# Kernel optimization log

Measured on AMD Instinct MI355X. Metric: run time of the kernel, lower is better.

The kernel has to match this reference:

```python
import jax, jax.numpy as jnp
import numpy as np

WS = 16      # window_size
HEADS = 8    # num_heads
EPS = 1e-5   # LayerNorm eps (torch default)


def setup_inputs() -> dict:
    key = jax.random.key(0)
    ks = jax.random.split(key, 7)
    C = 256
    x = jax.random.normal(ks[0], (8, C, 128, 128), dtype=jnp.float32)
    # LayerNorm params (torch init: weight=1, bias=0)
    ln_w = jnp.ones((C,), jnp.float32)
    ln_b = jnp.zeros((C,), jnp.float32)
    # MultiheadAttention in_proj (3C x C) and out_proj (C x C), xavier-ish scale
    s = 1.0 / np.sqrt(C)
    w_qkv = jax.random.uniform(ks[1], (3 * C, C), jnp.float32, -s, s)
    b_qkv = jnp.zeros((3 * C,), jnp.float32)
    w_out = jax.random.uniform(ks[2], (C, C), jnp.float32, -s, s)
    b_out = jnp.zeros((C,), jnp.float32)
    return {"x": x, "ln_w": ln_w, "ln_b": ln_b, "w_qkv": w_qkv,
            "b_qkv": b_qkv, "w_out": w_out, "b_out": b_out}


def _layernorm(x, w, b):
    mu = jnp.mean(x, axis=-1, keepdims=True)
    var = jnp.mean(jnp.square(x - mu), axis=-1, keepdims=True)
    return (x - mu) * jax.lax.rsqrt(var + EPS) * w + b


def reference(x, ln_w, ln_b, w_qkv, b_qkv, w_out, b_out):
    B, C, H, W = x.shape
    pad_h = (WS - H % WS) % WS
    pad_w = (WS - W % WS) % WS
    if pad_h or pad_w:
        x_p = jnp.pad(x, ((0, 0), (0, 0), (0, pad_h), (0, pad_w)))
    else:
        x_p = x
    nH, nW = x_p.shape[2] // WS, x_p.shape[3] // WS
    T = WS * WS
    # window partition: [B,C,H,W] -> [B*nH*nW, T, C]
    win = x_p.reshape(B, C, nH, WS, nW, WS)
    win = win.transpose(0, 2, 4, 3, 5, 1).reshape(B * nH * nW, T, C)

    xn = _layernorm(win, ln_w, ln_b)
    # QKV projection: [N,T,3C]
    qkv = jnp.einsum('ntc,dc->ntd', xn, w_qkv) + b_qkv
    q, k, v = jnp.split(qkv, 3, axis=-1)
    hd = C // HEADS
    N = win.shape[0]
    q = q.reshape(N, T, HEADS, hd).transpose(0, 2, 1, 3)  # [N,h,T,hd]
    k = k.reshape(N, T, HEADS, hd).transpose(0, 2, 1, 3)
    v = v.reshape(N, T, HEADS, hd).transpose(0, 2, 1, 3)
    scores = jnp.einsum('nhqd,nhkd->nhqk', q, k) / jnp.sqrt(jnp.asarray(hd, q.dtype))
    attn = jax.nn.softmax(scores, axis=-1)
    ctx = jnp.einsum('nhqk,nhkd->nhqd', attn, v)
    ctx = ctx.transpose(0, 2, 1, 3).reshape(N, T, C)
    attn_out = jnp.einsum('ntc,dc->ntd', ctx, w_out) + b_out

    win = win + attn_out
    # window reverse: [N,T,C] -> [B,C,H,W]
    out = win.reshape(B, nH, nW, WS, WS, C)
    out = out.transpose(0, 5, 1, 3, 2, 4).reshape(B, C, nH * WS, nW * WS)
    return out[:, :, :H, :W]
```

## Files before the change

### kernel.cpp

```cpp
#include <hip/hip_runtime.h>
#include <hip/hip_bf16.h>

#define CD    256
#define HW_   16384
#define WSZ   16
#define TT    256
#define NWIN  512
#define NHEADS 8
#define HDIM  32

typedef __hip_bfloat16 bf16;
typedef unsigned short ushort_t;
typedef __attribute__((ext_vector_type(8))) short bf16x8;
typedef __attribute__((ext_vector_type(4))) float f32x4;

__device__ __forceinline__ ushort_t f2bu(float v) {
    union { bf16 b; ushort_t u; } cv; cv.b = __float2bfloat16(v); return cv.u;
}

__device__ __forceinline__ float fexp2(float x) {
#if __has_builtin(__builtin_amdgcn_exp2f)
    return __builtin_amdgcn_exp2f(x);
#else
    return exp2f(x);
#endif
}

__global__ __launch_bounds__(256)
void convw_kernel(const float* __restrict__ wq, const float* __restrict__ wo,
                  bf16* __restrict__ wqb, bf16* __restrict__ wob)
{
    int i = blockIdx.x * 256 + threadIdx.x;
    if (i < 3 * CD * CD) wqb[i] = __float2bfloat16(wq[i]);
    int j = i - 3 * CD * CD;
    if (j >= 0 && j < CD * CD) wob[j] = __float2bfloat16(wo[j]);
}

__global__ __launch_bounds__(64)
void ln_kernel(const float* __restrict__ x, const float* __restrict__ lnw,
               const float* __restrict__ lnb, bf16* __restrict__ xn)
{
    __shared__ bf16 buf[64][72];

    const int blk = blockIdx.x;
    const int n = blk >> 2, q4 = blk & 3;
    const int t = q4 * 64 + threadIdx.x;
    const int b = n >> 6, r = n & 63;
    const int h0 = (r >> 3) * WSZ, w0 = (r & 7) * WSZ;
    const int ty = t >> 4, tx = t & 15;
    const float* px = x + (size_t)b * CD * HW_ + (size_t)(h0 + ty) * 128 + (w0 + tx);

    float s = 0.f, ss = 0.f;
    for (int c = 0; c < CD; ++c) { float v = px[(size_t)c * HW_]; s += v; ss += v * v; }
    const float mean = s * (1.f / CD);
    const float var  = ss * (1.f / CD) - mean * mean;
    const float rstd = rsqrtf(fmaxf(var, 0.f) + 1e-5f);

    const size_t gbase = ((size_t)n * TT + (size_t)q4 * 64) * CD;
    for (int cb = 0; cb < 4; ++cb) {
        __syncthreads();
        #pragma unroll
        for (int c8 = 0; c8 < 8; ++c8) {
            union { int4 q; ushort_t u[8]; } pk;
            #pragma unroll
            for (int j = 0; j < 8; ++j) {
                int c = cb * 64 + c8 * 8 + j;
                float v = px[(size_t)c * HW_];
                pk.u[j] = f2bu((v - mean) * rstd * lnw[c] + lnb[c]);
            }
            *(int4*)&buf[threadIdx.x][c8 * 8] = pk.q;
        }
        __syncthreads();
        for (int sl = threadIdx.x; sl < 512; sl += 64) {
            int row = sl >> 3, ch = sl & 7;
            *(int4*)&xn[gbase + (size_t)row * CD + cb * 64 + ch * 8] =
                *(const int4*)&buf[row][ch * 8];
        }
    }
}

__global__ __launch_bounds__(256, 2)
void attn_kernel(const bf16* __restrict__ xn, const bf16* __restrict__ wqb,
                 const float* __restrict__ bqkv, bf16* __restrict__ ctx)
{
    const int n = blockIdx.x, h = blockIdx.y;
    const int tid = threadIdx.x;
    const int wave = tid >> 6, lane = tid & 63;
    const int l16 = lane & 15, q16 = lane >> 4;

    __shared__ union {
        struct { bf16 xs[256][32]; bf16 ws[96][32]; } st;
        bf16 qp[256][40];
    } u;
    __shared__ bf16 ks[256][40];
    __shared__ bf16 vst[32][264];

    f32x4 acc[4][6];
    const f32x4 zero = {0.f, 0.f, 0.f, 0.f};
    #pragma unroll
    for (int mt = 0; mt < 4; ++mt)
        #pragma unroll
        for (int nt = 0; nt < 6; ++nt) acc[mt][nt] = zero;

    const size_t xbase = ((size_t)n * TT + tid) * CD;
    for (int kc = 0; kc < 8; ++kc) {
        __syncthreads();
        {
            const int4* src = (const int4*)(xn + xbase + kc * 32);
            int4* dst = (int4*)&u.st.xs[tid][0];
            #pragma unroll
            for (int i = 0; i < 4; ++i) dst[i] = src[i];
        }
        #pragma unroll
        for (int sl0 = 0; sl0 < 2; ++sl0) {
            int sl = sl0 * 256 + tid;
            if (sl < 384) {
                int row = sl >> 2, ch = sl & 3;
                int mat = row >> 5, j = row & 31;
                *(int4*)&u.st.ws[row][ch * 8] =
                    *(const int4*)(wqb + ((size_t)(mat * CD + h * HDIM + j)) * CD
                                   + (size_t)kc * 32 + ch * 8);
            }
        }
        __syncthreads();
        bf16x8 af[4], bg[6];
        #pragma unroll
        for (int mt = 0; mt < 4; ++mt)
            af[mt] = *(const bf16x8*)&u.st.xs[wave * 64 + mt * 16 + l16][q16 * 8];
        #pragma unroll
        for (int nt = 0; nt < 6; ++nt)
            bg[nt] = *(const bf16x8*)&u.st.ws[nt * 16 + l16][q16 * 8];
        #pragma unroll
        for (int mt = 0; mt < 4; ++mt)
            #pragma unroll
            for (int nt = 0; nt < 6; ++nt)
                acc[mt][nt] = __builtin_amdgcn_mfma_f32_16x16x32_bf16(
                                  af[mt], bg[nt], acc[mt][nt], 0, 0, 0);
    }
    __syncthreads();

    const float qscale2 = 0.2550348683f;
    #pragma unroll
    for (int nt = 0; nt < 6; ++nt) {
        const int mat = nt >> 1;
        const int j = ((nt & 1) << 4) | l16;
        const float bias = bqkv[mat * CD + h * HDIM + j];
        #pragma unroll
        for (int mt = 0; mt < 4; ++mt)
            #pragma unroll
            for (int rr = 0; rr < 4; ++rr) {
                int tok = wave * 64 + mt * 16 + q16 * 4 + rr;
                float v = acc[mt][nt][rr] + bias;
                if (mat == 0)      u.qp[tok][j] = __float2bfloat16(v * qscale2);
                else if (mat == 1) ks[tok][j]   = __float2bfloat16(v);
                else               vst[j][tok]  = __float2bfloat16(v);
            }
    }
    __syncthreads();

    bf16x8 aq[4];
    #pragma unroll
    for (int mt = 0; mt < 4; ++mt)
        aq[mt] = *(const bf16x8*)&u.qp[wave * 64 + mt * 16 + l16][q16 * 8];

    bf16x8 onesf;
    #pragma unroll
    for (int j = 0; j < 8; ++j) onesf[j] = (short)0x3F80;

    f32x4 acc_o[4][2];
    f32x4 acc_l[4];
    #pragma unroll
    for (int mt = 0; mt < 4; ++mt) {
        acc_o[mt][0] = zero; acc_o[mt][1] = zero; acc_l[mt] = zero;
    }

    for (int kc = 0; kc < 8; ++kc) {
        bf16x8 kb0 = *(const bf16x8*)&ks[kc * 32 + l16][q16 * 8];
        bf16x8 kb1 = *(const bf16x8*)&ks[kc * 32 + 16 + l16][q16 * 8];
        #pragma unroll
        for (int mt = 0; mt < 4; ++mt) {
            f32x4 sc0 = __builtin_amdgcn_mfma_f32_16x16x32_bf16(aq[mt], kb0, zero, 0, 0, 0);
            f32x4 sc1 = __builtin_amdgcn_mfma_f32_16x16x32_bf16(aq[mt], kb1, zero, 0, 0, 0);
            #pragma unroll
            for (int rr = 0; rr < 4; ++rr) {
                float p0 = fexp2(sc0[rr]);
                float p1 = fexp2(sc1[rr]);
                int row = wave * 64 + mt * 16 + q16 * 4 + rr;
                u.qp[row][l16]      = __float2bfloat16(p0);
                u.qp[row][16 + l16] = __float2bfloat16(p1);
            }
        }
        bf16x8 vb0 = *(const bf16x8*)&vst[l16][kc * 32 + q16 * 8];
        bf16x8 vb1 = *(const bf16x8*)&vst[16 + l16][kc * 32 + q16 * 8];
        #pragma unroll
        for (int mt = 0; mt < 4; ++mt) {
            bf16x8 ap = *(const bf16x8*)&u.qp[wave * 64 + mt * 16 + l16][q16 * 8];
            acc_o[mt][0] = __builtin_amdgcn_mfma_f32_16x16x32_bf16(ap, vb0, acc_o[mt][0], 0, 0, 0);
            acc_o[mt][1] = __builtin_amdgcn_mfma_f32_16x16x32_bf16(ap, vb1, acc_o[mt][1], 0, 0, 0);
            acc_l[mt]    = __builtin_amdgcn_mfma_f32_16x16x32_bf16(ap, onesf, acc_l[mt], 0, 0, 0);
        }
    }

    #pragma unroll
    for (int mt = 0; mt < 4; ++mt)
        #pragma unroll
        for (int rr = 0; rr < 4; ++rr) {
            const float inv_l = 1.f / acc_l[mt][rr];
            int tok = wave * 64 + mt * 16 + q16 * 4 + rr;
            size_t base = ((size_t)n * TT + tok) * CD + h * HDIM;
            ctx[base + l16]      = __float2bfloat16(acc_o[mt][0][rr] * inv_l);
            ctx[base + 16 + l16] = __float2bfloat16(acc_o[mt][1][rr] * inv_l);
        }
}

__global__ __launch_bounds__(256, 2)
void proj_kernel(const bf16* __restrict__ ctx, const bf16* __restrict__ wob,
                 const float* __restrict__ bout, const float* __restrict__ x,
                 float* __restrict__ out)
{
    const int mb = blockIdx.x, nb = blockIdx.y;
    const int tid = threadIdx.x;
    const int wave = tid >> 6, lane = tid & 63;
    const int l16 = lane & 15, q16 = lane >> 4;
    const int rowbase = (wave >> 1) * 64, colbase = (wave & 1) * 64;

    __shared__ union {
        struct { bf16 a[128][64]; bf16 b[128][64]; } st;
        bf16 c[128][129];
    } u;

    f32x4 acc[4][4];
    const f32x4 zero = {0.f, 0.f, 0.f, 0.f};
    #pragma unroll
    for (int mt = 0; mt < 4; ++mt)
        #pragma unroll
        for (int nt = 0; nt < 4; ++nt) acc[mt][nt] = zero;

    const size_t m0 = (size_t)mb * 128;
    for (int kc = 0; kc < 4; ++kc) {
        __syncthreads();
        #pragma unroll
        for (int p = 0; p < 4; ++p) {
            int sl = p * 256 + tid;
            int row = sl >> 3, ch = sl & 7;
            *(int4*)&u.st.a[row][ch * 8] =
                *(const int4*)(ctx + (m0 + row) * CD + kc * 64 + ch * 8);
            *(int4*)&u.st.b[row][ch * 8] =
                *(const int4*)(wob + ((size_t)(nb * 128 + row)) * CD + kc * 64 + ch * 8);
        }
        __syncthreads();
        #pragma unroll
        for (int kt = 0; kt < 2; ++kt) {
            bf16x8 af[4], bg[4];
            #pragma unroll
            for (int mt = 0; mt < 4; ++mt)
                af[mt] = *(const bf16x8*)&u.st.a[rowbase + mt * 16 + l16][kt * 32 + q16 * 8];
            #pragma unroll
            for (int nt = 0; nt < 4; ++nt)
                bg[nt] = *(const bf16x8*)&u.st.b[colbase + nt * 16 + l16][kt * 32 + q16 * 8];
            #pragma unroll
            for (int mt = 0; mt < 4; ++mt)
                #pragma unroll
                for (int nt = 0; nt < 4; ++nt)
                    acc[mt][nt] = __builtin_amdgcn_mfma_f32_16x16x32_bf16(
                                      af[mt], bg[nt], acc[mt][nt], 0, 0, 0);
        }
    }
    __syncthreads();

    #pragma unroll
    for (int mt = 0; mt < 4; ++mt)
        #pragma unroll
        for (int nt = 0; nt < 4; ++nt)
            #pragma unroll
            for (int rr = 0; rr < 4; ++rr)
                u.c[rowbase + mt * 16 + q16 * 4 + rr][colbase + nt * 16 + l16] =
                    __float2bfloat16(acc[mt][nt][rr]);
    __syncthreads();

    const int dg = tid >> 5;
    const int t0 = (tid & 31) * 4;
    for (int p = 0; p < 16; ++p) {
        int d = p * 8 + dg;
        int c = nb * 128 + d;
        size_t g = m0 + t0;
        int n = (int)(g >> 8), wt = (int)(g & 255);
        int b = n >> 6, r = n & 63;
        int h0 = (r >> 3) * WSZ, w0 = (r & 7) * WSZ;
        int ty = wt >> 4, tx = wt & 15;
        size_t addr = (size_t)b * CD * HW_ + (size_t)c * HW_
                    + (size_t)(h0 + ty) * 128 + w0 + tx;
        float bias = bout[c];
        float4 xr = *(const float4*)(x + addr);
        float4 ov;
        ov.x = __bfloat162float(u.c[t0 + 0][d]) + bias + xr.x;
        ov.y = __bfloat162float(u.c[t0 + 1][d]) + bias + xr.y;
        ov.z = __bfloat162float(u.c[t0 + 2][d]) + bias + xr.z;
        ov.w = __bfloat162float(u.c[t0 + 3][d]) + bias + xr.w;
        *(float4*)(out + addr) = ov;
    }
}

extern "C" void kernel_launch(void* const* d_in, const int* in_sizes, int n_in,
                              void* d_out, int out_size, void* d_ws, size_t ws_size,
                              hipStream_t stream)
{
    const float* x   = (const float*)d_in[0];
    const float* lnw = (const float*)d_in[1];
    const float* lnb = (const float*)d_in[2];
    const float* wq  = (const float*)d_in[3];
    const float* bq  = (const float*)d_in[4];
    const float* wo  = (const float*)d_in[5];
    const float* bo  = (const float*)d_in[6];
    float* out = (float*)d_out;

    bf16* ctx = (bf16*)d_ws;
    bf16* wqb = ctx + (size_t)NWIN * TT * CD;
    bf16* wob = wqb + (size_t)3 * CD * CD;
    bf16* xn  = (bf16*)d_out;

    hipLaunchKernelGGL(convw_kernel, dim3(1024),         dim3(256), 0, stream, wq, wo, wqb, wob);
    hipLaunchKernelGGL(ln_kernel,    dim3(2048),         dim3(64),  0, stream, x, lnw, lnb, xn);
    hipLaunchKernelGGL(attn_kernel,  dim3(NWIN, NHEADS), dim3(256), 0, stream, xn, wqb, bq, ctx);
    hipLaunchKernelGGL(proj_kernel,  dim3(1024, 2),      dim3(256), 0, stream, ctx, wob, bo, x, out);
}
```

Baseline: 570.9 us.

## Load QKV projection MFMA fragments directly from global, shrink LDS for occupancy

The QKV projection loop no longer stages the activation and weight tiles through shared memory. Each lane now reads its MFMA operand fragments straight from global memory through precomputed row pointers, which removes two barriers per k-chunk. Row padding in the q, k and transposed-v shared buffers drops from 40/264 to 36/260 elements, and the staging union is gone. Together these cut LDS use so launch bounds can request 3 blocks per CU. The costs are strided, less coalesced global reads with no prefetch or double buffering, and 8-byte-aligned rather than 16-byte-aligned LDS vector reads.

```diff
diff --git a/kernel.cpp b/kernel.cpp
--- a/kernel.cpp
+++ b/kernel.cpp
@@ -79,7 +79,7 @@
     }
 }
 
-__global__ __launch_bounds__(256, 2)
+__global__ __launch_bounds__(256, 3)
 void attn_kernel(const bf16* __restrict__ xn, const bf16* __restrict__ wqb,
                  const float* __restrict__ bqkv, bf16* __restrict__ ctx)
 {
@@ -88,12 +88,9 @@
     const int wave = tid >> 6, lane = tid & 63;
     const int l16 = lane & 15, q16 = lane >> 4;
 
-    __shared__ union {
-        struct { bf16 xs[256][32]; bf16 ws[96][32]; } st;
-        bf16 qp[256][40];
-    } u;
-    __shared__ bf16 ks[256][40];
-    __shared__ bf16 vst[32][264];
+    __shared__ bf16 qp[256][36];
+    __shared__ bf16 ks[256][36];
+    __shared__ bf16 vst[32][260];
 
     f32x4 acc[4][6];
     const f32x4 zero = {0.f, 0.f, 0.f, 0.f};
@@ -102,34 +99,26 @@
         #pragma unroll
         for (int nt = 0; nt < 6; ++nt) acc[mt][nt] = zero;
 
-    const size_t xbase = ((size_t)n * TT + tid) * CD;
+    const bf16* arow[4];
+    #pragma unroll
+    for (int mt = 0; mt < 4; ++mt)
+        arow[mt] = xn + ((size_t)n * TT + wave * 64 + mt * 16 + l16) * CD + q16 * 8;
+    const bf16* brow[6];
+    #pragma unroll
+    for (int nt = 0; nt < 6; ++nt) {
+        const int mat = nt >> 1;
+        const int j = ((nt & 1) << 4) | l16;
+        brow[nt] = wqb + ((size_t)(mat * CD + h * HDIM + j)) * CD + q16 * 8;
+    }
+
     for (int kc = 0; kc < 8; ++kc) {
-        __syncthreads();
-        {
-            const int4* src = (const int4*)(xn + xbase + kc * 32);
-            int4* dst = (int4*)&u.st.xs[tid][0];
-            #pragma unroll
-            for (int i = 0; i < 4; ++i) dst[i] = src[i];
-        }
-        #pragma unroll
-        for (int sl0 = 0; sl0 < 2; ++sl0) {
-            int sl = sl0 * 256 + tid;
-            if (sl < 384) {
-                int row = sl >> 2, ch = sl & 3;
-                int mat = row >> 5, j = row & 31;
-                *(int4*)&u.st.ws[row][ch * 8] =
-                    *(const int4*)(wqb + ((size_t)(mat * CD + h * HDIM + j)) * CD
-                                   + (size_t)kc * 32 + ch * 8);
-            }
-        }
-        __syncthreads();
         bf16x8 af[4], bg[6];
         #pragma unroll
         for (int mt = 0; mt < 4; ++mt)
-            af[mt] = *(const bf16x8*)&u.st.xs[wave * 64 + mt * 16 + l16][q16 * 8];
+            af[mt] = *(const bf16x8*)(arow[mt] + kc * 32);
         #pragma unroll
         for (int nt = 0; nt < 6; ++nt)
-            bg[nt] = *(const bf16x8*)&u.st.ws[nt * 16 + l16][q16 * 8];
+            bg[nt] = *(const bf16x8*)(brow[nt] + kc * 32);
         #pragma unroll
         for (int mt = 0; mt < 4; ++mt)
             #pragma unroll
@@ -137,7 +126,6 @@
                 acc[mt][nt] = __builtin_amdgcn_mfma_f32_16x16x32_bf16(
                                   af[mt], bg[nt], acc[mt][nt], 0, 0, 0);
     }
-    __syncthreads();
 
     const float qscale2 = 0.2550348683f;
     #pragma unroll
@@ -151,9 +139,9 @@
             for (int rr = 0; rr < 4; ++rr) {
                 int tok = wave * 64 + mt * 16 + q16 * 4 + rr;
                 float v = acc[mt][nt][rr] + bias;
-                if (mat == 0)      u.qp[tok][j] = __float2bfloat16(v * qscale2);
-                else if (mat == 1) ks[tok][j]   = __float2bfloat16(v);
-                else               vst[j][tok]  = __float2bfloat16(v);
+                if (mat == 0)      qp[tok][j]  = __float2bfloat16(v * qscale2);
+                else if (mat == 1) ks[tok][j]  = __float2bfloat16(v);
+                else               vst[j][tok] = __float2bfloat16(v);
             }
     }
     __syncthreads();
@@ -161,7 +149,7 @@
     bf16x8 aq[4];
     #pragma unroll
     for (int mt = 0; mt < 4; ++mt)
-        aq[mt] = *(const bf16x8*)&u.qp[wave * 64 + mt * 16 + l16][q16 * 8];
+        aq[mt] = *(const bf16x8*)&qp[wave * 64 + mt * 16 + l16][q16 * 8];
 
     bf16x8 onesf;
     #pragma unroll
@@ -186,15 +174,15 @@
                 float p0 = fexp2(sc0[rr]);
                 float p1 = fexp2(sc1[rr]);
                 int row = wave * 64 + mt * 16 + q16 * 4 + rr;
-                u.qp[row][l16]      = __float2bfloat16(p0);
-                u.qp[row][16 + l16] = __float2bfloat16(p1);
+                qp[row][l16]      = __float2bfloat16(p0);
+                qp[row][16 + l16] = __float2bfloat16(p1);
             }
         }
         bf16x8 vb0 = *(const bf16x8*)&vst[l16][kc * 32 + q16 * 8];
         bf16x8 vb1 = *(const bf16x8*)&vst[16 + l16][kc * 32 + q16 * 8];
         #pragma unroll
         for (int mt = 0; mt < 4; ++mt) {
-            bf16x8 ap = *(const bf16x8*)&u.qp[wave * 64 + mt * 16 + l16][q16 * 8];
+            bf16x8 ap = *(const bf16x8*)&qp[wave * 64 + mt * 16 + l16][q16 * 8];
             acc_o[mt][0] = __builtin_amdgcn_mfma_f32_16x16x32_bf16(ap, vb0, acc_o[mt][0], 0, 0, 0);
             acc_o[mt][1] = __builtin_amdgcn_mfma_f32_16x16x32_bf16(ap, vb1, acc_o[mt][1], 0, 0, 0);
             acc_l[mt]    = __builtin_amdgcn_mfma_f32_16x16x32_bf16(ap, onesf, acc_l[mt], 0, 0, 0);
```

Measured after the change: 568.2 us. About the same (-0.5%).
